# Performance work log

Measured on AMD Instinct MI355X. Metric: run time of the kernel, lower is better.

## Reference

```python
import jax, jax.numpy as jnp
import numpy as np

HEADS = 16
NEG = -1e9  # matches masked_fill(-1000000000.0)

def setup_inputs() -> dict:
    key = jax.random.key(0)
    ks = jax.random.split(key, 7)
    B, T, C = 2, 2048, 1024
    s = 1.0 / np.sqrt(C)
    return {
        "q": jax.random.normal(ks[0], (B, T, C), jnp.float32),
        "k": jax.random.normal(ks[1], (B, T, C), jnp.float32),
        "v": jax.random.normal(ks[2], (B, T, C), jnp.float32),
        "Wq": jax.random.normal(ks[3], (C, C), jnp.float32) * s,
        "Wk": jax.random.normal(ks[4], (C, C), jnp.float32) * s,
        "Wv": jax.random.normal(ks[5], (C, C), jnp.float32) * s,
        "Wo": jax.random.normal(ks[6], (C, C), jnp.float32) * s,
    }

def reference(q, k, v, Wq, Wk, Wv, Wo):
    B, T, C = q.shape
    h = HEADS
    dk = C // h
    # torch Linear (no bias): y = x @ W.T ; weight is [out, in]
    def proj(x, W):
        return (x @ W.T).reshape(B, T, h, dk).transpose(0, 2, 1, 3)  # [B,h,T,dk]
    qh, kh, vh = proj(q, Wq), proj(k, Wk), proj(v, Wv)
    scale = jnp.asarray(dk, q.dtype) ** 0.5
    scores = jnp.einsum('bhqd,bhkd->bhqk', qh / scale, kh)  # [B,h,T,T]
    causal = jnp.tril(jnp.ones((T, T), dtype=bool))
    scores = jnp.where(causal[None, None], scores, jnp.asarray(NEG, scores.dtype))
    attn = jax.nn.softmax(scores, axis=-1)
    out = jnp.einsum('bhqk,bhkd->bhqd', attn, vh)  # [B,h,T,dk]
    concat = out.transpose(0, 2, 1, 3).reshape(B, T, C)
    return concat @ Wo.T
```

## Files before the change

### kernel.cpp

```cpp
#include <hip/hip_runtime.h>
#include <hip/hip_bf16.h>

typedef __bf16 bf16x8 __attribute__((ext_vector_type(8)));
typedef float  f32x4  __attribute__((ext_vector_type(4)));
typedef unsigned short u16;

__device__ __forceinline__ u16 f2bf(float f) {
    __bf16 h = (__bf16)f;
    return __builtin_bit_cast(u16, h);
}

__device__ __forceinline__ f32x4 mfma16(bf16x8 a, bf16x8 b, f32x4 c) {
    return __builtin_amdgcn_mfma_f32_16x16x32_bf16(a, b, c, 0, 0, 0);
}

__device__ __forceinline__ bf16x8 cvt8(float4 a0, float4 a1) {
    bf16x8 u;
    u[0] = (__bf16)a0.x; u[1] = (__bf16)a0.y; u[2] = (__bf16)a0.z; u[3] = (__bf16)a0.w;
    u[4] = (__bf16)a1.x; u[5] = (__bf16)a1.y; u[6] = (__bf16)a1.z; u[7] = (__bf16)a1.w;
    return u;
}

__device__ __forceinline__ void gload16(const u16* g, u16* l) {
    __builtin_amdgcn_global_load_lds(
        (const __attribute__((address_space(1))) void*)g,
        (__attribute__((address_space(3))) void*)l, 16, 0, 0);
}

__global__ __launch_bounds__(256) void cvt7(const float* __restrict__ q,
                                            const float* __restrict__ k,
                                            const float* __restrict__ v,
                                            const float* __restrict__ Wq,
                                            const float* __restrict__ Wk,
                                            const float* __restrict__ Wv,
                                            const float* __restrict__ Wo,
                                            u16* __restrict__ dst) {
    const int t = blockIdx.x * 256 + threadIdx.x;
    const float* s;
    int o;
    if (t < 0x80000)       { s = q; o = t; }
    else if (t < 0x100000) { s = k; o = t - 0x80000; }
    else if (t < 0x180000) { s = v; o = t - 0x100000; }
    else {
        const int r = t - 0x180000;
        const int w = r >> 17;
        o = r & 0x1FFFF;
        s = (w == 0) ? Wq : (w == 1) ? Wk : (w == 2) ? Wv : Wo;
    }
    const int off = o * 8;
    float4 f0 = *(const float4*)(s + off);
    float4 f1 = *(const float4*)(s + off + 4);
    *(bf16x8*)(dst + (size_t)t * 8) = cvt8(f0, f1);
}

__global__ __launch_bounds__(512, 2) void gemm_qkv(const u16* __restrict__ qb,
                                                   const u16* __restrict__ kb,
                                                   const u16* __restrict__ vb,
                                                   const u16* __restrict__ Wb,
                                                   u16* __restrict__ Qp,
                                                   u16* __restrict__ Kp,
                                                   u16* __restrict__ Vt) {
    constexpr int K = 1024, N = 1024;
    __shared__ __align__(16) u16 As[2][256 * 64];
    __shared__ __align__(16) u16 Bs[2][256 * 64];

    const int tid  = threadIdx.x;
    const int lane = tid & 63;
    const int w    = tid >> 6;
    const int wr = w >> 2, wc = w & 3;
    const int wg    = (blockIdx.x & 7) * 24 + (blockIdx.x >> 3);
    const int which = wg >> 6;
    const int inner = wg & 63;
    const int m0 = (inner >> 2) * 256, n0 = (inner & 3) * 256;
    const int colg = lane & 15, rowg = lane >> 4;

    const u16* A = (which == 0) ? qb : (which == 1) ? kb : vb;
    const u16* W = Wb + ((size_t)which << 20);

    size_t soff[4];
    int dofs[4];
#pragma unroll
    for (int i = 0; i < 4; ++i) {
        const int c   = i * 512 + tid;
        const int row = c >> 3;
        const int s   = (c & 7) ^ (row & 7);
        soff[i] = (size_t)row * K + s * 8;
        dofs[i] = c * 8;
    }

    f32x4 acc[8][4];
#pragma unroll
    for (int i = 0; i < 8; ++i)
#pragma unroll
        for (int j = 0; j < 4; ++j) acc[i][j] = (f32x4){0.f, 0.f, 0.f, 0.f};

    const u16* Abase = A + (size_t)m0 * K;
    const u16* Bbase = W + (size_t)n0 * K;

#pragma unroll
    for (int i = 0; i < 4; ++i) {
        gload16(Abase + soff[i], &As[0][dofs[i]]);
        gload16(Bbase + soff[i], &Bs[0][dofs[i]]);
    }
    __syncthreads();

    int p = 0;
    for (int t = 0; t < 16; ++t) {
        if (t < 15) {
            const int kk = (t + 1) * 64;
#pragma unroll
            for (int i = 0; i < 4; ++i) {
                gload16(Abase + soff[i] + kk, &As[p ^ 1][dofs[i]]);
                gload16(Bbase + soff[i] + kk, &Bs[p ^ 1][dofs[i]]);
            }
        }
#pragma unroll
        for (int ks = 0; ks < 2; ++ks) {
            bf16x8 af[8], bfr[4];
#pragma unroll
            for (int mi = 0; mi < 8; ++mi) {
                const int row = wr * 128 + mi * 16 + colg;
                const int sl  = ((ks << 2) + rowg) ^ (row & 7);
                af[mi] = *(const bf16x8*)(&As[p][row * 64 + sl * 8]);
            }
#pragma unroll
            for (int ni = 0; ni < 4; ++ni) {
                const int row = wc * 64 + ni * 16 + colg;
                const int sl  = ((ks << 2) + rowg) ^ (row & 7);
                bfr[ni] = *(const bf16x8*)(&Bs[p][row * 64 + sl * 8]);
            }
#pragma unroll
            for (int mi = 0; mi < 8; ++mi)
#pragma unroll
                for (int ni = 0; ni < 4; ++ni)
                    acc[mi][ni] = mfma16(af[mi], bfr[ni], acc[mi][ni]);
        }
        __syncthreads();
        p ^= 1;
    }

    u16* Crm = (which == 0) ? Qp : Kp;
#pragma unroll
    for (int mi = 0; mi < 8; ++mi) {
#pragma unroll
        for (int ni = 0; ni < 4; ++ni) {
#pragma unroll
            for (int r = 0; r < 4; ++r) {
                const int row = m0 + wr * 128 + mi * 16 + rowg * 4 + r;
                const int col = n0 + wc * 64 + ni * 16 + colg;
                const float vv = acc[mi][ni][r];
                if (which < 2) {
                    Crm[(size_t)row * N + col] = f2bf(vv);
                } else {
                    const int b = row >> 11, tt = row & 2047;
                    const int h = col >> 6,  d = col & 63;
                    Vt[((size_t)((b * 16 + h) * 64 + d) << 11) + tt] = f2bf(vv);
                }
            }
        }
    }
}

__global__ __launch_bounds__(256) void gemm_out(const u16* __restrict__ Ap,
                                                const u16* __restrict__ W,
                                                float* __restrict__ Cp) {
    constexpr int K = 1024, N = 1024;
    __shared__ __align__(16) u16 As[2][2048];
    __shared__ __align__(16) u16 Bs[2][4096];

    const int tid  = threadIdx.x;
    const int lane = tid & 63;
    const int w    = tid >> 6;
    const int wr = w >> 1, wc = w & 1;
    const int wg = (blockIdx.x & 7) * 64 + (blockIdx.x >> 3);
    const int m0 = (wg >> 3) * 64, n0 = (wg & 7) * 128;
    const int colg = lane & 15, rowg = lane >> 4;

    const int rowA = tid >> 2, kcA = tid & 3;
    const size_t aoff = (size_t)(m0 + rowA) * K + kcA * 8;
    const int wiA = rowA * 32 + (kcA ^ ((rowA >> 1) & 3)) * 8;

    size_t boff[2];
    int wiB[2];
#pragma unroll
    for (int i = 0; i < 2; ++i) {
        const int c   = i * 256 + tid;
        const int row = c >> 2;
        const int kc  = c & 3;
        boff[i] = (size_t)(n0 + row) * K + kc * 8;
        wiB[i] = row * 32 + (kc ^ ((row >> 1) & 3)) * 8;
    }
    const int kcr   = rowg ^ ((colg >> 1) & 3);
    const int rbase = colg * 32 + kcr * 8;

    f32x4 acc[2][4];
#pragma unroll
    for (int i = 0; i < 2; ++i)
#pragma unroll
        for (int j = 0; j < 4; ++j) acc[i][j] = (f32x4){0.f, 0.f, 0.f, 0.f};

    uint4 av = *(const uint4*)(Ap + aoff);
    uint4 bv[2];
#pragma unroll
    for (int i = 0; i < 2; ++i) bv[i] = *(const uint4*)(W + boff[i]);
    *(uint4*)(&As[0][wiA]) = av;
#pragma unroll
    for (int i = 0; i < 2; ++i) *(uint4*)(&Bs[0][wiB[i]]) = bv[i];
    __syncthreads();

    int p = 0;
    for (int t = 0; t < 32; ++t) {
        if (t < 31) {
            const int kk = (t + 1) * 32;
            av = *(const uint4*)(Ap + aoff + kk);
#pragma unroll
            for (int i = 0; i < 2; ++i) bv[i] = *(const uint4*)(W + boff[i] + kk);
        }
        {
            bf16x8 af[2], bfr[4];
#pragma unroll
            for (int mi = 0; mi < 2; ++mi)
                af[mi] = *(const bf16x8*)(&As[p][(wr * 32 + mi * 16) * 32 + rbase]);
#pragma unroll
            for (int ni = 0; ni < 4; ++ni)
                bfr[ni] = *(const bf16x8*)(&Bs[p][(wc * 64 + ni * 16) * 32 + rbase]);
#pragma unroll
            for (int mi = 0; mi < 2; ++mi)
#pragma unroll
                for (int ni = 0; ni < 4; ++ni)
                    acc[mi][ni] = mfma16(af[mi], bfr[ni], acc[mi][ni]);
        }
        if (t < 31) {
            *(uint4*)(&As[p ^ 1][wiA]) = av;
#pragma unroll
            for (int i = 0; i < 2; ++i) *(uint4*)(&Bs[p ^ 1][wiB[i]]) = bv[i];
        }
        __syncthreads();
        p ^= 1;
    }

#pragma unroll
    for (int mi = 0; mi < 2; ++mi)
#pragma unroll
        for (int ni = 0; ni < 4; ++ni)
#pragma unroll
            for (int r = 0; r < 4; ++r) {
                const int row = m0 + wr * 32 + mi * 16 + rowg * 4 + r;
                const int col = n0 + wc * 64 + ni * 16 + colg;
                Cp[(size_t)row * N + col] = acc[mi][ni][r];
            }
}

constexpr float CEXP = 0.18033688011112042f;

__global__ __launch_bounds__(256) void attn_causal(const u16* __restrict__ Qp,
                                                   const u16* __restrict__ Kp,
                                                   const u16* __restrict__ Vt,
                                                   u16* __restrict__ concat) {
    constexpr int T = 2048, C = 1024;
    __shared__ __align__(16) u16 Ks[128 * 64];
    __shared__ __align__(16) u16 Vs[64 * 128];
    __shared__ __align__(16) u16 Pl[4][2048];

    const int tid  = threadIdx.x;
    const int lane = tid & 63;
    const int w    = tid >> 6;
    const int colg = lane & 15, rowg = lane >> 4;

    const int idx = blockIdx.x;
    const int xcd = idx & 7;
    const int i1  = idx >> 3;
    const int bh  = xcd * 4 + (i1 & 3);
    const int qg  = 31 - (i1 >> 2);
    const int b = bh >> 4, h = bh & 15;

    const int q0 = (qg * 4 + w) * 16;
    const int nt    = (q0 + 143) >> 7;
    const int ktmax = ((qg * 4 + 3) * 16 + 143) >> 7;

    const char* Kg = (const char*)(Kp + (size_t)(b * T) * C + h * 64);
    const char* Vg = (const char*)(Vt + ((size_t)(b * 16 + h) * 64) * T);
    char* Ksb = (char*)Ks;
    char* Vsb = (char*)Vs;
    char* Pw  = (char*)&Pl[w][0];

    const u16* Qb = Qp + (size_t)(b * T + q0 + colg) * C + h * 64;
    const bf16x8 qf0 = *(const bf16x8*)(Qb + rowg * 8);
    const bf16x8 qf1 = *(const bf16x8*)(Qb + 32 + rowg * 8);

    float mm = -1e30f, ll = 0.f;
    f32x4 O[4];
#pragma unroll
    for (int g = 0; g < 4; ++g) O[g] = (f32x4){0.f, 0.f, 0.f, 0.f};

    const int sw = (colg & 7) << 4;

    for (int kt = 0; kt < ktmax; ++kt) {
        const int kvb = kt * 128;
        uint4 kst[4], vst[4];
#pragma unroll
        for (int i2 = 0; i2 < 4; ++i2) {
            const int s  = i2 * 4096 + tid * 16;
            const int kv = s >> 7, ir = s & 127;
            kst[i2] = *(const uint4*)(Kg + (size_t)(kvb + kv) * 2048 + ir);
            const int d = s >> 8, irv = s & 255;
            vst[i2] = *(const uint4*)(Vg + (size_t)d * 4096 + (size_t)kvb * 2 + irv);
        }
#pragma unroll
        for (int i2 = 0; i2 < 4; ++i2) {
            const int s  = i2 * 4096 + tid * 16;
            const int kv = s >> 7;
            *(uint4*)(Ksb + (s ^ ((kv & 7) << 4))) = kst[i2];
            const int d = s >> 8;
            *(uint4*)(Vsb + (s ^ ((d & 7) << 4))) = vst[i2];
        }
        __syncthreads();

        if (kt < nt) {
            float pr[8][4];
#pragma unroll
            for (int sub = 0; sub < 8; ++sub) {
                const int kb = (sub * 16 + colg) * 128 + rowg * 16;
                bf16x8 kf0 = *(const bf16x8*)(Ksb + (kb ^ sw));
                bf16x8 kf1 = *(const bf16x8*)(Ksb + ((kb + 64) ^ sw));
                f32x4 t = (f32x4){0.f, 0.f, 0.f, 0.f};
                t = mfma16(kf0, qf0, t);
                t = mfma16(kf1, qf1, t);
#pragma unroll
                for (int r = 0; r < 4; ++r) pr[sub][r] = t[r];
            }
            if (kvb + 127 > q0) {
#pragma unroll
                for (int sub = 0; sub < 8; ++sub)
#pragma unroll
                    for (int r = 0; r < 4; ++r)
                        if (kvb + sub * 16 + rowg * 4 + r > q0 + colg) pr[sub][r] = -1e30f;
            }
            float mx[8];
#pragma unroll
            for (int sub = 0; sub < 8; ++sub)
                mx[sub] = fmaxf(fmaxf(pr[sub][0], pr[sub][1]), fmaxf(pr[sub][2], pr[sub][3]));
            float pm = fmaxf(fmaxf(fmaxf(mx[0], mx[1]), fmaxf(mx[2], mx[3])),
                             fmaxf(fmaxf(mx[4], mx[5]), fmaxf(mx[6], mx[7])));
            pm = fmaxf(pm, __shfl_xor(pm, 16, 64));
            pm = fmaxf(pm, __shfl_xor(pm, 32, 64));
            if (__any(pm > mm + 40.f)) {
                const float mn = fmaxf(mm, pm);
                const float sc = __builtin_amdgcn_exp2f((mm - mn) * CEXP);
                mm = mn;
                ll *= sc;
#pragma unroll
                for (int r = 0; r < 4; ++r) {
                    const float scr = __shfl(sc, (lane & 48) + rowg * 4 + r, 64);
#pragma unroll
                    for (int g = 0; g < 4; ++g) O[g][r] *= scr;
                }
            }
            float rs = 0.f;
#pragma unroll
            for (int sub = 0; sub < 8; ++sub) {
                const float e0 = __builtin_amdgcn_exp2f((pr[sub][0] - mm) * CEXP);
                const float e1 = __builtin_amdgcn_exp2f((pr[sub][1] - mm) * CEXP);
                const float e2 = __builtin_amdgcn_exp2f((pr[sub][2] - mm) * CEXP);
                const float e3 = __builtin_amdgcn_exp2f((pr[sub][3] - mm) * CEXP);
                pr[sub][0] = e0; pr[sub][1] = e1; pr[sub][2] = e2; pr[sub][3] = e3;
                rs += (e0 + e1) + (e2 + e3);
            }
            rs += __shfl_xor(rs, 16, 64);
            rs += __shfl_xor(rs, 32, 64);
            ll += rs;
#pragma unroll
            for (int sub = 0; sub < 8; ++sub) {
                uint2 pk;
                pk.x = (unsigned)f2bf(pr[sub][0]) | ((unsigned)f2bf(pr[sub][1]) << 16);
                pk.y = (unsigned)f2bf(pr[sub][2]) | ((unsigned)f2bf(pr[sub][3]) << 16);
                const int wb = (colg * 256 + sub * 32 + rowg * 8) ^ sw;
                *(uint2*)(Pw + wb) = pk;
            }
            bf16x8 pf[4];
#pragma unroll
            for (int kc = 0; kc < 4; ++kc)
                pf[kc] = *(const bf16x8*)(Pw + ((colg * 256 + kc * 64 + rowg * 16) ^ sw));
#pragma unroll
            for (int g = 0; g < 4; ++g) {
                const int vb0 = (g * 16 + colg) * 256 + rowg * 16;
#pragma unroll
                for (int kc = 0; kc < 4; ++kc) {
                    bf16x8 vf = *(const bf16x8*)(Vsb + ((vb0 + kc * 64) ^ sw));
                    O[g] = mfma16(pf[kc], vf, O[g]);
                }
            }
        }
        __syncthreads();
    }

#pragma unroll
    for (int r = 0; r < 4; ++r) {
        const float lr = __shfl(ll, (lane & 48) + rowg * 4 + r, 64);
        const float rc = 1.f / lr;
        const size_t base = (size_t)(b * T + q0 + rowg * 4 + r) * C + h * 64;
#pragma unroll
        for (int g = 0; g < 4; ++g)
            concat[base + g * 16 + colg] = f2bf(O[g][r] * rc);
    }
}

extern "C" void kernel_launch(void* const* d_in, const int* in_sizes, int n_in,
                              void* d_out, int out_size, void* d_ws, size_t ws_size,
                              hipStream_t stream) {
    const float* q  = (const float*)d_in[0];
    const float* k  = (const float*)d_in[1];
    const float* v  = (const float*)d_in[2];
    const float* Wq = (const float*)d_in[3];
    const float* Wk = (const float*)d_in[4];
    const float* Wv = (const float*)d_in[5];
    const float* Wo = (const float*)d_in[6];
    float* out = (float*)d_out;

    constexpr size_t NELEM = (size_t)4096 * 1024;
    constexpr size_t WSZ   = (size_t)1 << 20;
    u16* QB  = (u16*)d_ws;
    u16* KB  = QB + NELEM;
    u16* VB  = KB + NELEM;
    u16* Wbf = VB + NELEM;
    u16* Qp  = Wbf + 4 * WSZ;
    u16* Kp  = Qp + NELEM;
    u16* Vt  = Kp + NELEM;
    u16* Cc  = Vt + NELEM;

    cvt7<<<8192, 256, 0, stream>>>(q, k, v, Wq, Wk, Wv, Wo, QB);

    gemm_qkv<<<192, 512, 0, stream>>>(QB, KB, VB, Wbf, Qp, Kp, Vt);

    attn_causal<<<1024, 256, 0, stream>>>(Qp, Kp, Vt, Cc);

    gemm_out<<<512, 256, 0, stream>>>(Cc, Wbf + 3 * WSZ, out);
}
```

Before: 142.9 us.

## Fuse fp32-to-bf16 activation conversion into QKV GEMM A-tile loading

```diff
diff --git a/kernel.cpp b/kernel.cpp
--- a/kernel.cpp
+++ b/kernel.cpp
@@ -27,35 +27,23 @@
         (__attribute__((address_space(3))) void*)l, 16, 0, 0);
 }
 
-__global__ __launch_bounds__(256) void cvt7(const float* __restrict__ q,
-                                            const float* __restrict__ k,
-                                            const float* __restrict__ v,
-                                            const float* __restrict__ Wq,
-                                            const float* __restrict__ Wk,
-                                            const float* __restrict__ Wv,
-                                            const float* __restrict__ Wo,
+__global__ __launch_bounds__(256) void cvtW(const float* __restrict__ W0,
+                                            const float* __restrict__ W1,
+                                            const float* __restrict__ W2,
+                                            const float* __restrict__ W3,
                                             u16* __restrict__ dst) {
-    const int t = blockIdx.x * 256 + threadIdx.x;
-    const float* s;
-    int o;
-    if (t < 0x80000)       { s = q; o = t; }
-    else if (t < 0x100000) { s = k; o = t - 0x80000; }
-    else if (t < 0x180000) { s = v; o = t - 0x100000; }
-    else {
-        const int r = t - 0x180000;
-        const int w = r >> 17;
-        o = r & 0x1FFFF;
-        s = (w == 0) ? Wq : (w == 1) ? Wk : (w == 2) ? Wv : Wo;
-    }
-    const int off = o * 8;
+    const int t     = blockIdx.x * 256 + threadIdx.x;
+    const int which = t >> 17;
+    const int off   = (t & 0x1FFFF) * 8;
+    const float* s  = (which == 0) ? W0 : (which == 1) ? W1 : (which == 2) ? W2 : W3;
     float4 f0 = *(const float4*)(s + off);
     float4 f1 = *(const float4*)(s + off + 4);
-    *(bf16x8*)(dst + (size_t)t * 8) = cvt8(f0, f1);
-}
-
-__global__ __launch_bounds__(512, 2) void gemm_qkv(const u16* __restrict__ qb,
-                                                   const u16* __restrict__ kb,
-                                                   const u16* __restrict__ vb,
+    *(bf16x8*)(dst + ((size_t)which << 20) + off) = cvt8(f0, f1);
+}
+
+__global__ __launch_bounds__(512, 2) void gemm_qkv(const float* __restrict__ q,
+                                                   const float* __restrict__ k,
+                                                   const float* __restrict__ v,
                                                    const u16* __restrict__ Wb,
                                                    u16* __restrict__ Qp,
                                                    u16* __restrict__ Kp,
@@ -74,17 +62,18 @@
     const int m0 = (inner >> 2) * 256, n0 = (inner & 3) * 256;
     const int colg = lane & 15, rowg = lane >> 4;
 
-    const u16* A = (which == 0) ? qb : (which == 1) ? kb : vb;
-    const u16* W = Wb + ((size_t)which << 20);
-
-    size_t soff[4];
+    const float* A = (which == 0) ? q : (which == 1) ? k : v;
+    const u16*   W = Wb + ((size_t)which << 20);
+
+    size_t aoff[4], boff[4];
     int dofs[4];
 #pragma unroll
     for (int i = 0; i < 4; ++i) {
         const int c   = i * 512 + tid;
         const int row = c >> 3;
         const int s   = (c & 7) ^ (row & 7);
-        soff[i] = (size_t)row * K + s * 8;
+        aoff[i] = (size_t)row * K + s * 8;
+        boff[i] = (size_t)row * K + s * 8;
         dofs[i] = c * 8;
     }
 
@@ -94,14 +83,19 @@
 #pragma unroll
         for (int j = 0; j < 4; ++j) acc[i][j] = (f32x4){0.f, 0.f, 0.f, 0.f};
 
-    const u16* Abase = A + (size_t)m0 * K;
-    const u16* Bbase = W + (size_t)n0 * K;
-
+    const float* Abase = A + (size_t)m0 * K;
+    const u16*   Bbase = W + (size_t)n0 * K;
+
+    float4 a0[4], a1[4];
 #pragma unroll
     for (int i = 0; i < 4; ++i) {
-        gload16(Abase + soff[i], &As[0][dofs[i]]);
-        gload16(Bbase + soff[i], &Bs[0][dofs[i]]);
-    }
+        a0[i] = *(const float4*)(Abase + aoff[i]);
+        a1[i] = *(const float4*)(Abase + aoff[i] + 4);
+        gload16(Bbase + boff[i], &Bs[0][dofs[i]]);
+    }
+#pragma unroll
+    for (int i = 0; i < 4; ++i)
+        *(bf16x8*)(&As[0][dofs[i]]) = cvt8(a0[i], a1[i]);
     __syncthreads();
 
     int p = 0;
@@ -110,9 +104,12 @@
             const int kk = (t + 1) * 64;
 #pragma unroll
             for (int i = 0; i < 4; ++i) {
-                gload16(Abase + soff[i] + kk, &As[p ^ 1][dofs[i]]);
-                gload16(Bbase + soff[i] + kk, &Bs[p ^ 1][dofs[i]]);
-            }
+                a0[i] = *(const float4*)(Abase + aoff[i] + kk);
+                a1[i] = *(const float4*)(Abase + aoff[i] + kk + 4);
+            }
+#pragma unroll
+            for (int i = 0; i < 4; ++i)
+                gload16(Bbase + boff[i] + kk, &Bs[p ^ 1][dofs[i]]);
         }
 #pragma unroll
         for (int ks = 0; ks < 2; ++ks) {
@@ -134,6 +131,11 @@
 #pragma unroll
                 for (int ni = 0; ni < 4; ++ni)
                     acc[mi][ni] = mfma16(af[mi], bfr[ni], acc[mi][ni]);
+        }
+        if (t < 15) {
+#pragma unroll
+            for (int i = 0; i < 4; ++i)
+                *(bf16x8*)(&As[p ^ 1][dofs[i]]) = cvt8(a0[i], a1[i]);
         }
         __syncthreads();
         p ^= 1;
@@ -419,18 +421,15 @@
 
     constexpr size_t NELEM = (size_t)4096 * 1024;
     constexpr size_t WSZ   = (size_t)1 << 20;
-    u16* QB  = (u16*)d_ws;
-    u16* KB  = QB + NELEM;
-    u16* VB  = KB + NELEM;
-    u16* Wbf = VB + NELEM;
+    u16* Wbf = (u16*)d_ws;
     u16* Qp  = Wbf + 4 * WSZ;
     u16* Kp  = Qp + NELEM;
     u16* Vt  = Kp + NELEM;
     u16* Cc  = Vt + NELEM;
 
-    cvt7<<<8192, 256, 0, stream>>>(q, k, v, Wq, Wk, Wv, Wo, QB);
-
-    gemm_qkv<<<192, 512, 0, stream>>>(QB, KB, VB, Wbf, Qp, Kp, Vt);
+    cvtW<<<2048, 256, 0, stream>>>(Wq, Wk, Wv, Wo, Wbf);
+
+    gemm_qkv<<<192, 512, 0, stream>>>(q, k, v, Wbf, Qp, Kp, Vt);
 
     attn_causal<<<1024, 256, 0, stream>>>(Qp, Kp, Vt, Cc);
 
```

Result: slower. 146.0 us (+2.1%).
